# Kernel tuning notes

Hardware: AMD Instinct MI355X
Metric: run time of the kernel (lower is better)

## Reference

```python
import jax, jax.numpy as jnp
import numpy as np

N_BANDS = 5
B = 256
L = 800
T = N_BANDS * L            # concatenated length
N = T - (N_BANDS - 1) - 1  # = 3995; length after dropping pads, minus 1


def setup_inputs() -> dict:
    key = jax.random.key(0)
    k1, k2 = jax.random.split(key)
    # times in [0, 1000): n_bands tensors of [B, L], stacked -> [n_bands, B, L]
    input_times = jax.random.uniform(k1, (N_BANDS, B, L), dtype=jnp.float32) * 1000.0
    N_total = jax.random.randint(k2, (B,), N // 2, N + 1, dtype=jnp.int32)
    N_total = N_total.at[0].set(N)  # ensure max(N_total) == N (static shape)
    return {"input_times": input_times, "N_total": N_total}


def reference(input_times, N_total):
    # sort_times: concat the n_bands [B, L] tensors along axis 1, sort, drop pads
    concat = jnp.transpose(input_times, (1, 0, 2)).reshape(B, T)  # == concat along axis 1
    sorted_times = jnp.sort(concat, axis=1)[:, N_BANDS - 1:]      # [B, N+1]
    st = sorted_times[:, :N + 1]                                  # N = max(N_total) (static)

    # banded delta matrix [N, N+1]: row i has -1 at col i, +1 at col i+1
    delta = jnp.eye(N, N + 1, k=1, dtype=jnp.float32) - jnp.eye(N, N + 1, k=0, dtype=jnp.float32)

    # batched matvec (original tiles delta per batch; broadcasting is equivalent math)
    diffs = jnp.einsum('ij,bj->bi', delta, st)                    # [B, N]

    mask = (jnp.arange(N)[None, :] < N_total[:, None]).astype(jnp.float32)
    return (diffs * mask)[:, :, None]                             # [B, N, 1]
```

## Files before the change

kernel.cpp:

```cpp
#include <hip/hip_runtime.h>
#include <float.h>

#define NB 5
#define BB 256
#define LL 800
#define TT (NB * LL)
#define NN (TT - NB)

constexpr int BLOCK = 1024;
constexpr int NBUK  = 4096;
constexpr int NV4   = TT / 4;

__global__ __launch_bounds__(BLOCK)
void bucket_rank_diff4(const float* __restrict__ in,
                       const int* __restrict__ ntotal,
                       float* __restrict__ out)
{
    __shared__ __align__(16) float scat[TT];
    __shared__ __align__(16) float srt[TT + 8];
    __shared__ __align__(16) int   cnt[NBUK];
    __shared__ __align__(16) int   bstart[NBUK];
    __shared__ int wsum[16];

    const int b    = blockIdx.x;
    const int tid  = threadIdx.x;
    const int lane = tid & 63;
    const int wid  = tid >> 6;
    const bool active = (tid < NV4);
    const float scale = (float)NBUK / 1000.0f;

    float4 x4 = make_float4(0.f, 0.f, 0.f, 0.f);
    if (active) {
        int band = tid / 200;
        int l4   = tid - band * 200;
        x4 = *(reinterpret_cast<const float4*>(in + (band * BB + b) * LL) + l4);
    }
    const int nt = ntotal[b];

    *reinterpret_cast<int4*>(&cnt[tid * 4]) = make_int4(0, 0, 0, 0);
    __syncthreads();

    float v[4];
    int   g[4];
    int   off[4];
    if (active) {
        v[0] = x4.x; v[1] = x4.y; v[2] = x4.z; v[3] = x4.w;
        #pragma unroll
        for (int k = 0; k < 4; ++k) {
            int gg = (int)(v[k] * scale);
            gg = gg < 0 ? 0 : (gg > NBUK - 1 ? NBUK - 1 : gg);
            g[k]   = gg;
            off[k] = atomicAdd(&cnt[gg], 1);
        }
    } else {
        g[0] = g[1] = g[2] = g[3] = -1;
    }
    __syncthreads();

    int bc[4];
    #pragma unroll
    for (int k = 0; k < 4; ++k) bc[k] = (g[k] >= 0) ? cnt[g[k]] : 0;

    int4 cq = *reinterpret_cast<int4*>(&cnt[tid * 4]);
    int  c0 = cq.x, c1 = cq.y, c2 = cq.z, c3 = cq.w;
    int  s  = c0 + c1 + c2 + c3;
    int  inc = s;
    #pragma unroll
    for (int d = 1; d < 64; d <<= 1) {
        int t = __shfl_up(inc, d);
        if (lane >= d) inc += t;
    }
    if (lane == 63) wsum[wid] = inc;
    __syncthreads();
    int wo = 0;
    #pragma unroll
    for (int w = 0; w < 16; ++w) wo += (w < wid) ? wsum[w] : 0;
    int run = (inc - s) + wo;
    *reinterpret_cast<int4*>(&bstart[tid * 4]) =
        make_int4(run, run + c0, run + c0 + c1, run + c0 + c1 + c2);
    __syncthreads();

    int pbase[4];
    if (active) {
        #pragma unroll
        for (int k = 0; k < 4; ++k) {
            pbase[k] = bstart[g[k]];
            scat[pbase[k] + off[k]] = v[k];
        }
    }
    __syncthreads();

    if (active) {
        #pragma unroll
        for (int k = 0; k < 4; ++k) {
            int lo = pbase[k];
            if (bc[k] == 1) {
                srt[lo] = v[k];
            } else {
                float x = v[k];
                int   p = lo + off[k];
                int   r = lo;
                int   hi = lo + bc[k];
                for (int j = lo; j < hi; ++j) {
                    float w = scat[j];
                    if (w < x || (w == x && j < p)) ++r;
                }
                srt[r] = x;
            }
        }
    }
    __syncthreads();

    if (tid < 999) {
        int j0 = 4 + 4 * tid;
        float4 q0 = *reinterpret_cast<const float4*>(&srt[j0]);
        float4 q1 = *reinterpret_cast<const float4*>(&srt[j0 + 4]);
        float d0 = q0.y - q0.x;
        float d1 = q0.z - q0.y;
        float d2 = q0.w - q0.z;
        float d3 = q1.x - q0.w;
        int i0 = 4 * tid;
        float* o = out + b * NN + i0;
        o[0] = (i0     < nt) ? d0 : 0.0f;
        o[1] = (i0 + 1 < nt) ? d1 : 0.0f;
        o[2] = (i0 + 2 < nt) ? d2 : 0.0f;
        if (i0 + 3 < NN) o[3] = (i0 + 3 < nt) ? d3 : 0.0f;
    }
}

extern "C" void kernel_launch(void* const* d_in, const int* in_sizes, int n_in,
                              void* d_out, int out_size, void* d_ws, size_t ws_size,
                              hipStream_t stream) {
    const float* in  = (const float*)d_in[0];
    const int*   nt  = (const int*)d_in[1];
    float*       out = (float*)d_out;
    (void)in_sizes; (void)n_in; (void)out_size; (void)d_ws; (void)ws_size;
    bucket_rank_diff4<<<BB, BLOCK, 0, stream>>>(in, nt, out);
}
```

Baseline: 11.82 us.

## Double bucket count and rank small buckets with branchless 8-wide window compare

Raises the number of counting buckets from 4096 to 8192 so buckets hold fewer elements. Each block thread now scans 8 counters in the prefix sum. For buckets that fit in an aligned 8-element window, the rank comes from two float4 loads and an unrolled branchless compare, and the window is padded with FLT_MAX sentinels at the end of the array. This replaces the variable-length loop and its divergence. The trade-off is double the shared memory for cnt/bstart, which could reduce occupancy, and a longer per-thread scan.

```diff
diff --git a/kernel.cpp b/kernel.cpp
--- a/kernel.cpp
+++ b/kernel.cpp
@@ -8,15 +8,15 @@
 #define NN (TT - NB)
 
 constexpr int BLOCK = 1024;
-constexpr int NBUK  = 4096;
+constexpr int NBUK  = 8192;
 constexpr int NV4   = TT / 4;
 
 __global__ __launch_bounds__(BLOCK)
-void bucket_rank_diff4(const float* __restrict__ in,
+void bucket_wrank_diff(const float* __restrict__ in,
                        const int* __restrict__ ntotal,
                        float* __restrict__ out)
 {
-    __shared__ __align__(16) float scat[TT];
+    __shared__ __align__(16) float scat[TT + 8];
     __shared__ __align__(16) float srt[TT + 8];
     __shared__ __align__(16) int   cnt[NBUK];
     __shared__ __align__(16) int   bstart[NBUK];
@@ -37,7 +37,9 @@
     }
     const int nt = ntotal[b];
 
-    *reinterpret_cast<int4*>(&cnt[tid * 4]) = make_int4(0, 0, 0, 0);
+    *reinterpret_cast<int4*>(&cnt[tid * 8])     = make_int4(0, 0, 0, 0);
+    *reinterpret_cast<int4*>(&cnt[tid * 8 + 4]) = make_int4(0, 0, 0, 0);
+    if (tid < 8) scat[TT + tid] = FLT_MAX;
     __syncthreads();
 
     float v[4];
@@ -61,10 +63,13 @@
     #pragma unroll
     for (int k = 0; k < 4; ++k) bc[k] = (g[k] >= 0) ? cnt[g[k]] : 0;
 
-    int4 cq = *reinterpret_cast<int4*>(&cnt[tid * 4]);
-    int  c0 = cq.x, c1 = cq.y, c2 = cq.z, c3 = cq.w;
-    int  s  = c0 + c1 + c2 + c3;
-    int  inc = s;
+    int4 q0 = *reinterpret_cast<int4*>(&cnt[tid * 8]);
+    int4 q1 = *reinterpret_cast<int4*>(&cnt[tid * 8 + 4]);
+    int c[8] = {q0.x, q0.y, q0.z, q0.w, q1.x, q1.y, q1.z, q1.w};
+    int s = 0;
+    #pragma unroll
+    for (int k = 0; k < 8; ++k) s += c[k];
+    int inc = s;
     #pragma unroll
     for (int d = 1; d < 64; d <<= 1) {
         int t = __shfl_up(inc, d);
@@ -76,8 +81,11 @@
     #pragma unroll
     for (int w = 0; w < 16; ++w) wo += (w < wid) ? wsum[w] : 0;
     int run = (inc - s) + wo;
-    *reinterpret_cast<int4*>(&bstart[tid * 4]) =
-        make_int4(run, run + c0, run + c0 + c1, run + c0 + c1 + c2);
+    int bs[8];
+    #pragma unroll
+    for (int k = 0; k < 8; ++k) { bs[k] = run; run += c[k]; }
+    *reinterpret_cast<int4*>(&bstart[tid * 8])     = make_int4(bs[0], bs[1], bs[2], bs[3]);
+    *reinterpret_cast<int4*>(&bstart[tid * 8 + 4]) = make_int4(bs[4], bs[5], bs[6], bs[7]);
     __syncthreads();
 
     int pbase[4];
@@ -93,14 +101,23 @@
     if (active) {
         #pragma unroll
         for (int k = 0; k < 4; ++k) {
-            int lo = pbase[k];
-            if (bc[k] == 1) {
-                srt[lo] = v[k];
+            int   lo = pbase[k];
+            float x  = v[k];
+            int   p  = lo + off[k];
+            int   wb = lo & ~3;
+            if ((lo & 3) + bc[k] <= 8) {
+                float4 a = *reinterpret_cast<const float4*>(&scat[wb]);
+                float4 d = *reinterpret_cast<const float4*>(&scat[wb + 4]);
+                float ws8[8] = {a.x, a.y, a.z, a.w, d.x, d.y, d.z, d.w};
+                int r = wb;
+                #pragma unroll
+                for (int t = 0; t < 8; ++t) {
+                    int j = wb + t;
+                    r += (ws8[t] < x || (ws8[t] == x && j < p)) ? 1 : 0;
+                }
+                srt[r] = x;
             } else {
-                float x = v[k];
-                int   p = lo + off[k];
-                int   r = lo;
-                int   hi = lo + bc[k];
+                int r = lo, hi = lo + bc[k];
                 for (int j = lo; j < hi; ++j) {
                     float w = scat[j];
                     if (w < x || (w == x && j < p)) ++r;
@@ -113,12 +130,12 @@
 
     if (tid < 999) {
         int j0 = 4 + 4 * tid;
-        float4 q0 = *reinterpret_cast<const float4*>(&srt[j0]);
-        float4 q1 = *reinterpret_cast<const float4*>(&srt[j0 + 4]);
-        float d0 = q0.y - q0.x;
-        float d1 = q0.z - q0.y;
-        float d2 = q0.w - q0.z;
-        float d3 = q1.x - q0.w;
+        float4 p0 = *reinterpret_cast<const float4*>(&srt[j0]);
+        float4 p1 = *reinterpret_cast<const float4*>(&srt[j0 + 4]);
+        float d0 = p0.y - p0.x;
+        float d1 = p0.z - p0.y;
+        float d2 = p0.w - p0.z;
+        float d3 = p1.x - p0.w;
         int i0 = 4 * tid;
         float* o = out + b * NN + i0;
         o[0] = (i0     < nt) ? d0 : 0.0f;
@@ -135,5 +152,5 @@
     const int*   nt  = (const int*)d_in[1];
     float*       out = (float*)d_out;
     (void)in_sizes; (void)n_in; (void)out_size; (void)d_ws; (void)ws_size;
-    bucket_rank_diff4<<<BB, BLOCK, 0, stream>>>(in, nt, out);
+    bucket_wrank_diff<<<BB, BLOCK, 0, stream>>>(in, nt, out);
 }
```

New measurement: 11.52 us. -2.6%, faster.

## Use fixed-capacity padded buckets to rank within buckets before prefix scan

Applied to the files above, without the earlier changes.

Replaces the count/scan/scatter/rank sequence with fixed-capacity buckets of 12 slots (2048 buckets), where each element is written directly into its bucket slot during the atomic pass. The within-bucket rank is computed from three float4 loads before the prefix scan, which removes one scatter pass and one barrier and overlaps the ranking with the scan. Buckets that overflow spill into a small shared overflow list, capped at 64 entries. This adds FLT_MAX initialisation of a 96KB padded buffer and raises shared memory use. The results are wrong if more than 64 elements overflow.

```diff
diff --git a/kernel.cpp b/kernel.cpp
--- a/kernel.cpp
+++ b/kernel.cpp
@@ -8,19 +8,24 @@
 #define NN (TT - NB)
 
 constexpr int BLOCK = 1024;
-constexpr int NBUK  = 4096;
+constexpr int NBUK  = 2048;
+constexpr int CAP   = 12;
 constexpr int NV4   = TT / 4;
+constexpr int OVFMX = 64;
 
 __global__ __launch_bounds__(BLOCK)
-void bucket_rank_diff4(const float* __restrict__ in,
-                       const int* __restrict__ ntotal,
-                       float* __restrict__ out)
+void padded_bucket_diff(const float* __restrict__ in,
+                        const int* __restrict__ ntotal,
+                        float* __restrict__ out)
 {
-    __shared__ __align__(16) float scat[TT];
+    __shared__ __align__(16) float pscat[NBUK * CAP];
     __shared__ __align__(16) float srt[TT + 8];
     __shared__ __align__(16) int   cnt[NBUK];
     __shared__ __align__(16) int   bstart[NBUK];
-    __shared__ int wsum[16];
+    __shared__ int   wsum[16];
+    __shared__ int   novf;
+    __shared__ float ovf_v[OVFMX];
+    __shared__ int   ovf_g[OVFMX];
 
     const int b    = blockIdx.x;
     const int tid  = threadIdx.x;
@@ -37,7 +42,12 @@
     }
     const int nt = ntotal[b];
 
-    *reinterpret_cast<int4*>(&cnt[tid * 4]) = make_int4(0, 0, 0, 0);
+    *reinterpret_cast<int2*>(&cnt[tid * 2]) = make_int2(0, 0);
+    const float4 fm4 = make_float4(FLT_MAX, FLT_MAX, FLT_MAX, FLT_MAX);
+    #pragma unroll
+    for (int k = 0; k < (NBUK * CAP) / (BLOCK * 4); ++k)
+        *reinterpret_cast<float4*>(&pscat[tid * 4 + k * (BLOCK * 4)]) = fm4;
+    if (tid == 0) novf = 0;
     __syncthreads();
 
     float v[4];
@@ -49,21 +59,58 @@
         for (int k = 0; k < 4; ++k) {
             int gg = (int)(v[k] * scale);
             gg = gg < 0 ? 0 : (gg > NBUK - 1 ? NBUK - 1 : gg);
-            g[k]   = gg;
-            off[k] = atomicAdd(&cnt[gg], 1);
+            g[k] = gg;
+            int o = atomicAdd(&cnt[gg], 1);
+            if (o < CAP) {
+                pscat[gg * CAP + o] = v[k];
+                off[k] = o;
+            } else {
+                int oi = atomicAdd(&novf, 1);
+                if (oi < OVFMX) { ovf_v[oi] = v[k]; ovf_g[oi] = gg; }
+                off[k] = CAP + oi;
+            }
         }
     } else {
         g[0] = g[1] = g[2] = g[3] = -1;
     }
     __syncthreads();
 
-    int bc[4];
-    #pragma unroll
-    for (int k = 0; k < 4; ++k) bc[k] = (g[k] >= 0) ? cnt[g[k]] : 0;
-
-    int4 cq = *reinterpret_cast<int4*>(&cnt[tid * 4]);
-    int  c0 = cq.x, c1 = cq.y, c2 = cq.z, c3 = cq.w;
-    int  s  = c0 + c1 + c2 + c3;
+    const int nov = novf;
+    int rb[4];
+    if (active) {
+        #pragma unroll
+        for (int k = 0; k < 4; ++k) {
+            const float* wp = &pscat[g[k] * CAP];
+            float4 a = *reinterpret_cast<const float4*>(wp);
+            float4 c = *reinterpret_cast<const float4*>(wp + 4);
+            float4 d = *reinterpret_cast<const float4*>(wp + 8);
+            float w12[12] = {a.x, a.y, a.z, a.w, c.x, c.y, c.z, c.w, d.x, d.y, d.z, d.w};
+            float x = v[k];
+            int   r = 0;
+            if (off[k] < CAP) {
+                int p = off[k];
+                #pragma unroll
+                for (int j = 0; j < CAP; ++j)
+                    r += (w12[j] < x || (w12[j] == x && j < p)) ? 1 : 0;
+                if (nov > 0)
+                    for (int i = 0; i < nov && i < OVFMX; ++i)
+                        if (ovf_g[i] == g[k]) r += (ovf_v[i] < x) ? 1 : 0;
+            } else {
+                int myi = off[k] - CAP;
+                #pragma unroll
+                for (int j = 0; j < CAP; ++j)
+                    r += (w12[j] <= x) ? 1 : 0;
+                for (int i = 0; i < nov && i < OVFMX; ++i)
+                    if (i != myi && ovf_g[i] == g[k]) {
+                        float w = ovf_v[i];
+                        r += (w < x || (w == x && i < myi)) ? 1 : 0;
+                    }
+            }
+            rb[k] = r;
+        }
+    }
+    int2 cc = *reinterpret_cast<int2*>(&cnt[tid * 2]);
+    int  s  = cc.x + cc.y;
     int  inc = s;
     #pragma unroll
     for (int d = 1; d < 64; d <<= 1) {
@@ -76,49 +123,24 @@
     #pragma unroll
     for (int w = 0; w < 16; ++w) wo += (w < wid) ? wsum[w] : 0;
     int run = (inc - s) + wo;
-    *reinterpret_cast<int4*>(&bstart[tid * 4]) =
-        make_int4(run, run + c0, run + c0 + c1, run + c0 + c1 + c2);
-    __syncthreads();
-
-    int pbase[4];
-    if (active) {
-        #pragma unroll
-        for (int k = 0; k < 4; ++k) {
-            pbase[k] = bstart[g[k]];
-            scat[pbase[k] + off[k]] = v[k];
-        }
-    }
+    *reinterpret_cast<int2*>(&bstart[tid * 2]) = make_int2(run, run + cc.x);
     __syncthreads();
 
     if (active) {
         #pragma unroll
-        for (int k = 0; k < 4; ++k) {
-            int lo = pbase[k];
-            if (bc[k] == 1) {
-                srt[lo] = v[k];
-            } else {
-                float x = v[k];
-                int   p = lo + off[k];
-                int   r = lo;
-                int   hi = lo + bc[k];
-                for (int j = lo; j < hi; ++j) {
-                    float w = scat[j];
-                    if (w < x || (w == x && j < p)) ++r;
-                }
-                srt[r] = x;
-            }
-        }
+        for (int k = 0; k < 4; ++k)
+            srt[bstart[g[k]] + rb[k]] = v[k];
     }
     __syncthreads();
 
     if (tid < 999) {
         int j0 = 4 + 4 * tid;
-        float4 q0 = *reinterpret_cast<const float4*>(&srt[j0]);
-        float4 q1 = *reinterpret_cast<const float4*>(&srt[j0 + 4]);
-        float d0 = q0.y - q0.x;
-        float d1 = q0.z - q0.y;
-        float d2 = q0.w - q0.z;
-        float d3 = q1.x - q0.w;
+        float4 p0 = *reinterpret_cast<const float4*>(&srt[j0]);
+        float4 p1 = *reinterpret_cast<const float4*>(&srt[j0 + 4]);
+        float d0 = p0.y - p0.x;
+        float d1 = p0.z - p0.y;
+        float d2 = p0.w - p0.z;
+        float d3 = p1.x - p0.w;
         int i0 = 4 * tid;
         float* o = out + b * NN + i0;
         o[0] = (i0     < nt) ? d0 : 0.0f;
@@ -135,5 +157,5 @@
     const int*   nt  = (const int*)d_in[1];
     float*       out = (float*)d_out;
     (void)in_sizes; (void)n_in; (void)out_size; (void)d_ws; (void)ws_size;
-    bucket_rank_diff4<<<BB, BLOCK, 0, stream>>>(in, nt, out);
+    padded_bucket_diff<<<BB, BLOCK, 0, stream>>>(in, nt, out);
 }
```

Result: no change. 11.90 us (+0.7%).
